# Kernel tuning notes

Hardware: AMD Instinct MI355X
Metric: run time of the kernel (lower is better)

Reference implementation:

```python
import jax, jax.numpy as jnp
import numpy as np
from jax import lax

B, D_MODEL, H, W = 8, 384, 64, 64
D_INNER, D_STATE, D_CONV, DT_RANK = 768, 16, 4, 24
C3, MLP_H = 3 * D_MODEL, 4 * D_MODEL
EPS = 1e-5


def setup_inputs():
    key = jax.random.key(0)
    ks = jax.random.split(key, 16)
    r = lambda i, shape, s=0.02: jax.random.normal(ks[i], shape, jnp.float32) * s
    return {
        'x': jax.random.normal(ks[0], (B, D_MODEL, H, W), jnp.float32),
        'ln1_g': jnp.ones((D_MODEL,), jnp.float32), 'ln1_b': jnp.zeros((D_MODEL,), jnp.float32),
        'in_w': r(1, (2 * D_INNER, D_MODEL)),
        'conv_w': r(2, (D_INNER, 1, D_CONV), 0.2), 'conv_b': jnp.zeros((D_INNER,), jnp.float32),
        'xproj_w': r(3, (DT_RANK + 2 * D_STATE, D_INNER)),
        'dtproj_w': r(4, (D_INNER, DT_RANK), 0.1),
        'dtproj_b': jnp.full((D_INNER,), jnp.log(jnp.expm1(0.01)).item(), jnp.float32),
        'A_log': jnp.log(jnp.broadcast_to(jnp.arange(1, D_STATE + 1, dtype=jnp.float32), (D_INNER, D_STATE))),
        'Dskip': jnp.ones((D_INNER,), jnp.float32),
        'out_w': r(5, (D_MODEL, D_INNER)),
        'dw_w': r(6, (C3, 1, 3, 3), 0.1),
        'bn_g': jnp.ones((C3,), jnp.float32), 'bn_b': jnp.zeros((C3,), jnp.float32),
        'bn_mean': jnp.zeros((C3,), jnp.float32), 'bn_var': jnp.ones((C3,), jnp.float32),
        'pw_w': r(7, (C3, C3)),
        'fus_w': r(8, (D_MODEL, D_MODEL)), 'fus_b': jnp.zeros((D_MODEL,), jnp.float32),
        'ln2_g': jnp.ones((D_MODEL,), jnp.float32), 'ln2_b': jnp.zeros((D_MODEL,), jnp.float32),
        'mlp_w1': r(9, (MLP_H, D_MODEL)), 'mlp_b1': jnp.zeros((MLP_H,), jnp.float32),
        'mlp_w2': r(10, (D_MODEL, MLP_H)), 'mlp_b2': jnp.zeros((D_MODEL,), jnp.float32),
    }


def _ln(x, g, b):
    m = x.mean(-1, keepdims=True)
    v = ((x - m) ** 2).mean(-1, keepdims=True)
    return (x - m) / jnp.sqrt(v + EPS) * g + b


def _dwt(x):
    x01 = x[:, :, 0::2, :] / 2
    x02 = x[:, :, 1::2, :] / 2
    x1, x3 = x01[:, :, :, 0::2], x01[:, :, :, 1::2]
    x2, x4 = x02[:, :, :, 0::2], x02[:, :, :, 1::2]
    ll = x1 + x2 + x3 + x4
    hl = -x1 - x2 + x3 + x4
    lh = -x1 + x2 - x3 + x4
    hh = x1 - x2 - x3 + x4
    return ll, jnp.concatenate([hl, lh, hh], axis=1)


def _idwt(ll, high):
    b, c, h, w = ll.shape
    hl, lh, hh = jnp.split(high, 3, axis=1)
    h_ll, h_hl, h_lh, h_hh = ll / 2, hl / 2, lh / 2, hh / 2
    y1 = h_ll - h_hl - h_lh + h_hh  # (even row, even col)
    y2 = h_ll - h_hl + h_lh - h_hh  # (odd row, even col)
    y3 = h_ll + h_hl - h_lh - h_hh  # (even row, odd col)
    y4 = h_ll + h_hl + h_lh + h_hh  # (odd row, odd col)
    row_e = jnp.stack([y1, y3], axis=-1).reshape(b, c, h, 2 * w)
    row_o = jnp.stack([y2, y4], axis=-1).reshape(b, c, h, 2 * w)
    return jnp.stack([row_e, row_o], axis=-2).reshape(b, c, 2 * h, 2 * w)


def _mamba(x, in_w, conv_w, conv_b, xproj_w, dtproj_w, dtproj_b, A_log, Dskip, out_w):
    # x: [B, L, d_model]
    bb = x.shape[0]
    xz = x @ in_w.T  # [B,L,2*d_inner]
    xi, z = jnp.split(xz, 2, axis=-1)
    xc = jnp.swapaxes(xi, 1, 2)  # [B,d_inner,L]
    xc = lax.conv_general_dilated(xc, conv_w, (1,), [(D_CONV - 1, 0)],
                                  feature_group_count=D_INNER,
                                  dimension_numbers=('NCH', 'OIH', 'NCH')) + conv_b[None, :, None]
    u = jax.nn.silu(jnp.swapaxes(xc, 1, 2))  # [B,L,d_inner]
    dbl = u @ xproj_w.T
    dtr = dbl[..., :DT_RANK]
    Bm = dbl[..., DT_RANK:DT_RANK + D_STATE]
    Cm = dbl[..., DT_RANK + D_STATE:]
    dt = jax.nn.softplus(dtr @ dtproj_w.T + dtproj_b)  # [B,L,d_inner]
    A = -jnp.exp(A_log)  # [d_inner,d_state]

    def step(h, t):
        dt_t, B_t, C_t, u_t = t
        dA = jnp.exp(dt_t[:, :, None] * A)
        h = dA * h + (dt_t * u_t)[:, :, None] * B_t[:, None, :]
        return h, jnp.sum(h * C_t[:, None, :], axis=-1)

    h0 = jnp.zeros((bb, D_INNER, D_STATE), x.dtype)
    xs = (jnp.swapaxes(dt, 0, 1), jnp.swapaxes(Bm, 0, 1), jnp.swapaxes(Cm, 0, 1), jnp.swapaxes(u, 0, 1))
    _, ys = lax.scan(step, h0, xs)
    y = jnp.swapaxes(ys, 0, 1) + u * Dskip
    y = y * jax.nn.silu(z)
    return y @ out_w.T


def reference(x, ln1_g, ln1_b, in_w, conv_w, conv_b, xproj_w, dtproj_w, dtproj_b,
              A_log, Dskip, out_w, dw_w, bn_g, bn_b, bn_mean, bn_var, pw_w,
              fus_w, fus_b, ln2_g, ln2_b, mlp_w1, mlp_b1, mlp_w2, mlp_b2):
    shortcut = x
    x_ll, x_high = _dwt(x)
    b, c, hh, ww = x_ll.shape
    # LL branch: LN -> Mamba -> residual
    x_ll_in = _ln(jnp.transpose(x_ll, (0, 2, 3, 1)), ln1_g, ln1_b)
    y = _mamba(x_ll_in.reshape(b, hh * ww, c), in_w, conv_w, conv_b, xproj_w,
               dtproj_w, dtproj_b, A_log, Dskip, out_w)
    x_ll_out = x_ll + jnp.transpose(y.reshape(b, hh, ww, c), (0, 3, 1, 2))
    # High-freq branch: depthwise3x3 -> BN(eval) -> SiLU -> 1x1 -> residual
    hd = lax.conv_general_dilated(x_high, dw_w, (1, 1), [(1, 1), (1, 1)],
                                  feature_group_count=C3,
                                  dimension_numbers=('NCHW', 'OIHW', 'NCHW'))
    hd = (hd - bn_mean[None, :, None, None]) / jnp.sqrt(bn_var + EPS)[None, :, None, None] \
         * bn_g[None, :, None, None] + bn_b[None, :, None, None]
    hd = jax.nn.silu(hd)
    x_high_out = x_high + jnp.einsum('bchw,oc->bohw', hd, pw_w)
    # Reconstruct + fusion 1x1 conv + residual
    recon = _idwt(x_ll_out, x_high_out)
    recon = jnp.einsum('bchw,oc->bohw', recon, fus_w) + fus_b[None, :, None, None]
    x2 = shortcut + recon
    # LN + MLP + residual
    xn = _ln(jnp.transpose(x2, (0, 2, 3, 1)), ln2_g, ln2_b)
    m = jax.nn.gelu(xn @ mlp_w1.T + mlp_b1, approximate=False) @ mlp_w2.T + mlp_b2
    return x2 + jnp.transpose(m, (0, 3, 1, 2))
```

## Files before the change

### kernel.cpp

```cpp
#include <hip/hip_runtime.h>
#include <hip/hip_bf16.h>
#include <math.h>

typedef __hip_bfloat16 bf16;
typedef __attribute__((ext_vector_type(8))) short bf16x8;
typedef __attribute__((ext_vector_type(4))) float f32x4;
typedef unsigned short u16;

#define LN_EPS 1e-5f

__device__ inline u16 f2b(float v) {
    __hip_bfloat16 h = __float2bfloat16(v);
    return *reinterpret_cast<u16*>(&h);
}

__device__ inline float b2f_lo(unsigned int w) { return __uint_as_float(w << 16); }
__device__ inline float b2f_hi(unsigned int w) { return __uint_as_float(w & 0xFFFF0000u); }

__device__ inline void gload_lds16(const void* g, void* l) {
    __builtin_amdgcn_global_load_lds(
        (const __attribute__((address_space(1))) void*)(uintptr_t)g,
        (__attribute__((address_space(3))) void*)(uintptr_t)(unsigned int)(uintptr_t)l,
        16, 0, 0);
}

__global__ __launch_bounds__(256) void sentinel_kernel(float* __restrict__ out, int n) {
    int i = blockIdx.x * 256 + threadIdx.x;
    if (i < n) out[i] = 123.0f;
}

__global__ __launch_bounds__(256) void reduce12_kernel(const float* __restrict__ P,
                                                       float* __restrict__ out, int n4) {
    int i = blockIdx.x * 256 + threadIdx.x;
    if (i >= n4) return;
    const float4* p4 = (const float4*)P;
    float4 s = p4[i];
#pragma unroll
    for (int z = 1; z < 12; z++) {
        float4 v = p4[(size_t)z * n4 + i];
        s.x += v.x; s.y += v.y; s.z += v.z; s.w += v.w;
    }
    ((float4*)out)[i] = s;
}

__global__ void detect_kernel(const unsigned int* __restrict__ g, int* __restrict__ flag) {
    *flag = (*g == 0x3F803F80u) ? 1 : 0;
}

struct Jobs {
    const void* src[25];
    int prefix[26];
};
__global__ __launch_bounds__(256) void convert_kernel(Jobs J, u16* __restrict__ dst16,
                                                      float* __restrict__ dst32,
                                                      const int* __restrict__ flag) {
    int i = blockIdx.x * 256 + threadIdx.x;
    int total = J.prefix[25];
    if (i >= total) return;
    int f = *flag;
    int lo = 0;
    while (J.prefix[lo + 1] <= i) lo++;
    int off = i - J.prefix[lo];
    float v = f ? (float)((const bf16*)J.src[lo])[off] : ((const float*)J.src[lo])[off];
    if (lo < 6) dst16[i] = f2b(v);
    else        dst32[i - J.prefix[6]] = v;
}

__global__ __launch_bounds__(256) void dwt_kernel(const void* __restrict__ xv,
                                                  float* __restrict__ xll,
                                                  float* __restrict__ xhigh,
                                                  const int* __restrict__ flag) {
    __shared__ float tile[32][133];
    int blk = blockIdx.x;
    int cc = blk % 12;
    int t2 = blk / 12;
    int i  = t2 % 32;
    int b  = t2 / 32;
    int t  = threadIdx.x;
    int c_l = t >> 3;
    int sub = t & 7;
    size_t rowbase = ((size_t)(b * 384 + cc * 32 + c_l)) * 4096 + (size_t)i * 128;
    if (*flag) {
        const u16* xp = (const u16*)xv + rowbase;
#pragma unroll
        for (int k = 0; k < 2; k++) {
            int e0 = (sub + k * 8) * 8;
            uint4 v = *(const uint4*)(xp + e0);
            tile[c_l][e0 + 0] = b2f_lo(v.x); tile[c_l][e0 + 1] = b2f_hi(v.x);
            tile[c_l][e0 + 2] = b2f_lo(v.y); tile[c_l][e0 + 3] = b2f_hi(v.y);
            tile[c_l][e0 + 4] = b2f_lo(v.z); tile[c_l][e0 + 5] = b2f_hi(v.z);
            tile[c_l][e0 + 6] = b2f_lo(v.w); tile[c_l][e0 + 7] = b2f_hi(v.w);
        }
    } else {
        const float* xp = (const float*)xv + rowbase;
#pragma unroll
        for (int k = 0; k < 4; k++) {
            int f0 = (sub + k * 8) * 4;
            float4 v = *(const float4*)(xp + f0);
            tile[c_l][f0 + 0] = v.x; tile[c_l][f0 + 1] = v.y;
            tile[c_l][f0 + 2] = v.z; tile[c_l][f0 + 3] = v.w;
        }
    }
    __syncthreads();
    int c_out = t & 31;
    int jg = t >> 5;
    int cg = cc * 32 + c_out;
#pragma unroll
    for (int jj = 0; jj < 4; jj++) {
        int j = jg * 4 + jj;
        float A = tile[c_out][2 * j];
        float B = tile[c_out][2 * j + 1];
        float C = tile[c_out][64 + 2 * j];
        float D = tile[c_out][64 + 2 * j + 1];
        float ll = 0.5f * (A + B + C + D);
        float hl = 0.5f * (B + D - A - C);
        float lh = 0.5f * (C + D - A - B);
        float hh = 0.5f * (A + D - B - C);
        int pm = b * 1024 + i * 32 + j;
        xll[(size_t)pm * 384 + cg] = ll;
        size_t hb = (size_t)pm * 1152;
        xhigh[hb + cg] = hl;
        xhigh[hb + 384 + cg] = lh;
        xhigh[hb + 768 + cg] = hh;
    }
}

template <bool OBF>
__global__ __launch_bounds__(128) void ln_kernel(const float* __restrict__ in,
                                                 void* __restrict__ outv,
                                                 const float* __restrict__ g,
                                                 const float* __restrict__ b) {
    const int C = 384;
    int row = blockIdx.x;
    int t = threadIdx.x;
    const float* rp = in + (size_t)row * C;
    float v0 = rp[t], v1 = rp[t + 128], v2 = rp[t + 256];
    __shared__ float red[128];
    red[t] = v0 + v1 + v2;
    __syncthreads();
    for (int off = 64; off > 0; off >>= 1) {
        if (t < off) red[t] += red[t + off];
        __syncthreads();
    }
    float mean = red[0] * (1.f / 384.f);
    __syncthreads();
    float d0 = v0 - mean, d1 = v1 - mean, d2 = v2 - mean;
    red[t] = d0 * d0 + d1 * d1 + d2 * d2;
    __syncthreads();
    for (int off = 64; off > 0; off >>= 1) {
        if (t < off) red[t] += red[t + off];
        __syncthreads();
    }
    float inv = rsqrtf(red[0] * (1.f / 384.f) + LN_EPS);
    float o0 = d0 * inv * g[t]       + b[t];
    float o1 = d1 * inv * g[t + 128] + b[t + 128];
    float o2 = d2 * inv * g[t + 256] + b[t + 256];
    if constexpr (OBF) {
        u16* op = (u16*)outv + (size_t)row * C;
        op[t] = f2b(o0); op[t + 128] = f2b(o1); op[t + 256] = f2b(o2);
    } else {
        float* op = (float*)outv + (size_t)row * C;
        op[t] = o0; op[t + 128] = o1; op[t + 256] = o2;
    }
}

#define EP_NONE 0
#define EP_SOFTPLUS_BIAS 1
#define EP_ADD 2
#define EP_FUS 3
#define EP_GELU_BIAS 4
#define EP_FINAL 5

template <int EPIL, bool CBF>
__global__ __launch_bounds__(256) void gemm_mfma(const u16* __restrict__ A, int lda,
                                                 const u16* __restrict__ W,
                                                 void* __restrict__ Cp, int ldc,
                                                 int M, int N, int K,
                                                 const float* __restrict__ addsrc,
                                                 const float* __restrict__ bias,
                                                 const void* __restrict__ xres,
                                                 void* __restrict__ obf,
                                                 int m_off,
                                                 const int* __restrict__ flag) {
    __shared__ u16 Als[2][128][32];
    __shared__ u16 Bls[2][128][32];
    const int t = threadIdx.x;
    const int wave = t >> 6, lane = t & 63;
    const int quad = lane >> 4, r16 = lane & 15;
    const int wm = (wave >> 1) * 64, wn = (wave & 1) * 64;
    const int mb = blockIdx.y * 128, nb = blockIdx.x * 128;
    f32x4 acc[4][4] = {};

    const int srow = wave * 32 + (lane >> 2);
    const int scol = (lane & 3) * 8;
    const u16* Ag0 = A + (size_t)(mb + srow) * lda + scol;
    const u16* Ag1 = A + (size_t)(mb + srow + 16) * lda + scol;
    const u16* Wg0 = W + (size_t)(nb + srow) * (size_t)K + scol;
    const u16* Wg1 = W + (size_t)(nb + srow + 16) * (size_t)K + scol;

    gload_lds16(Ag0, &Als[0][wave * 32][0]);
    gload_lds16(Ag1, &Als[0][wave * 32 + 16][0]);
    gload_lds16(Wg0, &Bls[0][wave * 32][0]);
    gload_lds16(Wg1, &Bls[0][wave * 32 + 16][0]);
    __syncthreads();

    int cur = 0;
    for (int k0 = 0; k0 < K; k0 += 32) {
        int nxt = cur ^ 1;
        if (k0 + 32 < K) {
            gload_lds16(Ag0 + k0 + 32, &Als[nxt][wave * 32][0]);
            gload_lds16(Ag1 + k0 + 32, &Als[nxt][wave * 32 + 16][0]);
            gload_lds16(Wg0 + k0 + 32, &Bls[nxt][wave * 32][0]);
            gload_lds16(Wg1 + k0 + 32, &Bls[nxt][wave * 32 + 16][0]);
        }
        bf16x8 af[4], bfv[4];
#pragma unroll
        for (int i = 0; i < 4; i++) af[i] = *(const bf16x8*)&Als[cur][wm + i * 16 + r16][quad * 8];
#pragma unroll
        for (int j = 0; j < 4; j++) bfv[j] = *(const bf16x8*)&Bls[cur][wn + j * 16 + r16][quad * 8];
#pragma unroll
        for (int i = 0; i < 4; i++)
#pragma unroll
            for (int j = 0; j < 4; j++)
                acc[i][j] = __builtin_amdgcn_mfma_f32_16x16x32_bf16(af[i], bfv[j], acc[i][j], 0, 0, 0);
        __syncthreads();
        cur = nxt;
    }

    int f = 0;
    if constexpr (EPIL == EP_FUS || EPIL == EP_FINAL) f = *flag;
#pragma unroll
    for (int i = 0; i < 4; i++) {
#pragma unroll
        for (int j = 0; j < 4; j++) {
#pragma unroll
            for (int rg = 0; rg < 4; rg++) {
                int m = mb + wm + i * 16 + quad * 4 + rg;
                int n = nb + wn + j * 16 + r16;
                float v = acc[i][j][rg];
                if constexpr (EPIL == EP_NONE) {
                    if constexpr (CBF) ((u16*)Cp)[(size_t)m * ldc + n] = f2b(v);
                    else               ((float*)Cp)[(size_t)m * ldc + n] = v;
                } else if constexpr (EPIL == EP_ADD) {
                    ((float*)Cp)[(size_t)m * ldc + n] = addsrc[(size_t)m * ldc + n] + v;
                } else if constexpr (EPIL == EP_FUS) {
                    v += bias[n];
                    int bb = m >> 12, pix = m & 4095;
                    size_t xi = ((size_t)(bb * 384 + n) << 12) + pix;
                    v += f ? (float)((const bf16*)xres)[xi] : ((const float*)xres)[xi];
                    ((float*)Cp)[(size_t)m * ldc + n] = v;
                } else if constexpr (EPIL == EP_GELU_BIAS) {
                    v += bias[n];
                    v = 0.5f * v * (1.f + erff(v * 0.70710678118654752f));
                    if constexpr (CBF) ((u16*)Cp)[(size_t)m * ldc + n] = f2b(v);
                    else               ((float*)Cp)[(size_t)m * ldc + n] = v;
                } else if constexpr (EPIL == EP_FINAL) {
                    v += bias[n];
                    int gm = m_off + m;
                    v += addsrc[(size_t)gm * 384 + n];
                    int bb = gm >> 12, pix = gm & 4095;
                    size_t oi = ((size_t)(bb * 384 + n) << 12) + pix;
                    if (f) ((bf16*)obf)[oi] = __float2bfloat16(v);
                    else   ((float*)obf)[oi] = v;
                }
            }
        }
    }
}

template <int EPIL, bool SPLITK>
__global__ __launch_bounds__(256) void gemm_nt(const float* __restrict__ A, int lda,
                                               const float* __restrict__ W,
                                               float* __restrict__ C, int ldc,
                                               int M, int N, int K,
                                               const float* __restrict__ bias,
                                               int kc) {
    __shared__ __align__(16) float As[16][68];
    __shared__ __align__(16) float Bs[16][68];
    int t = threadIdx.x;
    int mb = blockIdx.y * 64;
    int nb = blockIdx.x * 64;
    int kb = SPLITK ? blockIdx.z * kc : 0;
    int ke = SPLITK ? kb + kc : K;
    int tm = t & 15, tn = t >> 4;
    float* Cout = C;
    if constexpr (SPLITK) Cout = C + (size_t)blockIdx.z * (size_t)M * ldc;
    float acc[4][4] = {};
    for (int k0 = kb; k0 < ke; k0 += 16) {
#pragma unroll
        for (int i = 0; i < 4; i++) {
            int idx = t + i * 256;
            int r = idx >> 4, c = idx & 15;
            float v = 0.f;
            if (k0 + c < K) v = A[(size_t)(mb + r) * lda + k0 + c];
            As[c][r] = v;
        }
#pragma unroll
        for (int i = 0; i < 4; i++) {
            int idx = t + i * 256;
            int r = idx >> 4, c = idx & 15;
            float v = 0.f;
            if ((nb + r) < N && (k0 + c) < K) v = W[(size_t)(nb + r) * K + k0 + c];
            Bs[c][r] = v;
        }
        __syncthreads();
#pragma unroll
        for (int kk = 0; kk < 16; kk++) {
            float4 av = *(const float4*)&As[kk][tm * 4];
            float4 bv = *(const float4*)&Bs[kk][tn * 4];
            float a4[4] = {av.x, av.y, av.z, av.w};
            float b4[4] = {bv.x, bv.y, bv.z, bv.w};
#pragma unroll
            for (int i = 0; i < 4; i++)
#pragma unroll
                for (int j = 0; j < 4; j++) acc[i][j] += a4[i] * b4[j];
        }
        __syncthreads();
    }
#pragma unroll
    for (int i = 0; i < 4; i++) {
        int m = mb + tm * 4 + i;
        if (m >= M) continue;
#pragma unroll
        for (int j = 0; j < 4; j++) {
            int n = nb + tn * 4 + j;
            if (n >= N) continue;
            float v = acc[i][j];
            if constexpr (SPLITK) {
                Cout[(size_t)m * ldc + n] = v;
            } else if constexpr (EPIL == EP_NONE) {
                C[(size_t)m * ldc + n] = v;
            } else if constexpr (EPIL == EP_SOFTPLUS_BIAS) {
                v += bias[n];
                v = (v > 20.f) ? v : log1pf(expf(v));
                C[(size_t)m * ldc + n] = v;
            }
        }
    }
}

__global__ __launch_bounds__(256) void conv1d_silu_kernel(const float* __restrict__ xz,
                                                          const float* __restrict__ cw,
                                                          const float* __restrict__ cb,
                                                          float* __restrict__ u) {
    int tid = blockIdx.x * 256 + threadIdx.x;
    int dq = tid % 192;
    int t2 = tid / 192;
    int l = t2 % 1024;
    int b = t2 / 1024;
    int d = dq * 4;
    float4 q0 = *(const float4*)&cw[d * 4];
    float4 q1 = *(const float4*)&cw[d * 4 + 4];
    float4 q2 = *(const float4*)&cw[d * 4 + 8];
    float4 q3 = *(const float4*)&cw[d * 4 + 12];
    float4 acc = *(const float4*)&cb[d];
    int rowbase = b * 1024;
#pragma unroll
    for (int k = 0; k < 4; k++) {
        int ls = l - 3 + k;
        if (ls < 0) continue;
        float4 xv = *(const float4*)&xz[(size_t)(rowbase + ls) * 1536 + d];
        acc.x += ((const float*)&q0)[k] * xv.x;
        acc.y += ((const float*)&q1)[k] * xv.y;
        acc.z += ((const float*)&q2)[k] * xv.z;
        acc.w += ((const float*)&q3)[k] * xv.w;
    }
    float4 o;
    o.x = acc.x / (1.f + __expf(-acc.x));
    o.y = acc.y / (1.f + __expf(-acc.y));
    o.z = acc.z / (1.f + __expf(-acc.z));
    o.w = acc.w / (1.f + __expf(-acc.w));
    *(float4*)&u[(size_t)(rowbase + l) * 768 + d] = o;
}

__device__ inline void scan_load_ac(const float* __restrict__ A_log, int d,
                                    float (&Ac)[16], bool& structured) {
#pragma unroll
    for (int s = 0; s < 16; s++) Ac[s] = -__expf(A_log[d * 16 + s]);
    structured = true;
#pragma unroll
    for (int s = 0; s < 16; s++)
        structured = structured && (fabsf(Ac[s] - (s + 1) * Ac[0]) <= 1e-5f * fabsf(Ac[s]));
}

__global__ __launch_bounds__(256) void scan_p1(const float* __restrict__ dt,
                                               const float* __restrict__ u,
                                               const float* __restrict__ dbl,
                                               const float* __restrict__ A_log,
                                               float* __restrict__ st) {
    __shared__ float Bsh[8][16];
    int tloc = threadIdx.x;
    int idx = blockIdx.x * 256 + tloc;
    int g = idx % 6144;
    int c = idx / 6144;
    int d = g % 768, b = g / 768;
    float Ac[16]; bool structured;
    scan_load_ac(A_log, d, Ac, structured);
    float h[16];
#pragma unroll
    for (int s = 0; s < 16; s++) h[s] = 0.f;
    float S = 0.f;
    size_t m0 = (size_t)b * 1024 + c * 128;
    for (int j0 = 0; j0 < 128; j0 += 8) {
        __syncthreads();
        if (tloc < 128) {
            int jj = tloc >> 4, ff = tloc & 15;
            Bsh[jj][ff] = dbl[(m0 + j0 + jj) * 56 + 24 + ff];
        }
        __syncthreads();
        if (structured) {
#pragma unroll
            for (int j = 0; j < 8; j++) {
                size_t m = m0 + j0 + j;
                float dtv = dt[m * 768 + d];
                float uv  = u[m * 768 + d];
                float du = dtv * uv;
                S += dtv;
                float q = __expf(dtv * Ac[0]);
                float a = q;
                h[0] = a * h[0] + du * Bsh[j][0];
#pragma unroll
                for (int s = 1; s < 16; s++) { a *= q; h[s] = a * h[s] + du * Bsh[j][s]; }
            }
        } else {
#pragma unroll
            for (int j = 0; j < 8; j++) {
                size_t m = m0 + j0 + j;
                float dtv = dt[m * 768 + d];
                float uv  = u[m * 768 + d];
                float du = dtv * uv;
                S += dtv;
#pragma unroll
                for (int s = 0; s < 16; s++) h[s] = __expf(dtv * Ac[s]) * h[s] + du * Bsh[j][s];
            }
        }
    }
    float* stp = st + (size_t)(c * 6144 + g) * 32;
#pragma unroll
    for (int s = 0; s < 16; s++) stp[s] = __expf(Ac[s] * S);
#pragma unroll
    for (int s = 0; s < 16; s++) stp[16 + s] = h[s];
}

__global__ __launch_bounds__(256) void scan_p2(float* __restrict__ st) {
    int tid = blockIdx.x * 256 + threadIdx.x;
    int s = tid & 15;
    int g = tid >> 4;
    float H = 0.f;
#pragma unroll
    for (int c = 0; c < 8; c++) {
        size_t i = (size_t)(c * 6144 + g) * 32;
        float P  = st[i + s];
        float hE = st[i + 16 + s];
        st[i + s] = H;
        H = hE + P * H;
    }
}

__global__ __launch_bounds__(256) void scan_p3(const float* __restrict__ dt,
                                               const float* __restrict__ u,
                                               const float* __restrict__ dbl,
                                               const float* __restrict__ z,
                                               const float* __restrict__ A_log,
                                               const float* __restrict__ Dskip,
                                               const float* __restrict__ st,
                                               u16* __restrict__ ybuf) {
    __shared__ float BCsh[8][32];
    int tloc = threadIdx.x;
    int idx = blockIdx.x * 256 + tloc;
    int g = idx % 6144;
    int c = idx / 6144;
    int d = g % 768, b = g / 768;
    float Ac[16]; bool structured;
    scan_load_ac(A_log, d, Ac, structured);
    float Dsk = Dskip[d];
    float h[16];
    const float* stp = st + (size_t)(c * 6144 + g) * 32;
#pragma unroll
    for (int s = 0; s < 16; s++) h[s] = stp[s];
    size_t m0 = (size_t)b * 1024 + c * 128;
    for (int j0 = 0; j0 < 128; j0 += 8) {
        __syncthreads();
        {
            int jj = tloc >> 5, ff = tloc & 31;
            BCsh[jj][ff] = dbl[(m0 + j0 + jj) * 56 + 24 + ff];
        }
        __syncthreads();
        if (structured) {
#pragma unroll
            for (int j = 0; j < 8; j++) {
                size_t m = m0 + j0 + j;
                float dtv = dt[m * 768 + d];
                float uv  = u[m * 768 + d];
                float zv  = z[m * 1536 + 768 + d];
                float du = dtv * uv;
                float q = __expf(dtv * Ac[0]);
                float a = q;
                h[0] = a * h[0] + du * BCsh[j][0];
                float y = h[0] * BCsh[j][16];
#pragma unroll
                for (int s = 1; s < 16; s++) {
                    a *= q;
                    h[s] = a * h[s] + du * BCsh[j][s];
                    y += h[s] * BCsh[j][16 + s];
                }
                float sig = 1.f / (1.f + __expf(-zv));
                ybuf[m * 3072 + d] = f2b((y + uv * Dsk) * (zv * sig));
            }
        } else {
#pragma unroll
            for (int j = 0; j < 8; j++) {
                size_t m = m0 + j0 + j;
                float dtv = dt[m * 768 + d];
                float uv  = u[m * 768 + d];
                float zv  = z[m * 1536 + 768 + d];
                float du = dtv * uv;
                float y = 0.f;
#pragma unroll
                for (int s = 0; s < 16; s++) {
                    h[s] = __expf(dtv * Ac[s]) * h[s] + du * BCsh[j][s];
                    y += h[s] * BCsh[j][16 + s];
                }
                float sig = 1.f / (1.f + __expf(-zv));
                ybuf[m * 3072 + d] = f2b((y + uv * Dsk) * (zv * sig));
            }
        }
    }
}

__global__ __launch_bounds__(256) void dwconv_bn_silu_kernel(const float* __restrict__ xh,
                                                             const float* __restrict__ w,
                                                             const float* __restrict__ g,
                                                             const float* __restrict__ bb,
                                                             const float* __restrict__ mean,
                                                             const float* __restrict__ var,
                                                             u16* __restrict__ hd) {
    int tid = blockIdx.x * 256 + threadIdx.x;
    int cq = tid % 288;
    int t2 = tid / 288;
    int xc = t2 & 3;
    int t3 = t2 >> 2;
    int y = t3 % 32;
    int b = t3 / 32;
    int c = cq * 4;
    float wk[9][4];
#pragma unroll
    for (int i = 0; i < 4; i++) {
        float4 wa = *(const float4*)&w[(c + i) * 9];
        float4 wbv = *(const float4*)&w[(c + i) * 9 + 4];
        float wcv = w[(c + i) * 9 + 8];
        wk[0][i] = wa.x; wk[1][i] = wa.y; wk[2][i] = wa.z; wk[3][i] = wa.w;
        wk[4][i] = wbv.x; wk[5][i] = wbv.y; wk[6][i] = wbv.z; wk[7][i] = wbv.w;
        wk[8][i] = wcv;
    }
    float4 mn = *(const float4*)&mean[c];
    float4 vr = *(const float4*)&var[c];
    float4 gg = *(const float4*)&g[c];
    float4 bv = *(const float4*)&bb[c];
    float scl[4], sft[4];
    scl[0] = rsqrtf(vr.x + LN_EPS) * gg.x; sft[0] = bv.x - mn.x * scl[0];
    scl[1] = rsqrtf(vr.y + LN_EPS) * gg.y; sft[1] = bv.y - mn.y * scl[1];
    scl[2] = rsqrtf(vr.z + LN_EPS) * gg.z; sft[2] = bv.z - mn.z * scl[2];
    scl[3] = rsqrtf(vr.w + LN_EPS) * gg.w; sft[3] = bv.w - mn.w * scl[3];

    int x0 = xc * 8;
    size_t pixbase = (size_t)b * 1024 + y * 32;
    float win[3][3][4];
    auto ldcol = [&](int xx, float (&col)[3][4]) {
#pragma unroll
        for (int r = 0; r < 3; r++) {
            int yy = y + r - 1;
            if (xx < 0 || xx > 31 || yy < 0 || yy > 31) {
                col[r][0] = col[r][1] = col[r][2] = col[r][3] = 0.f;
            } else {
                float4 v = *(const float4*)&xh[((size_t)b * 1024 + yy * 32 + xx) * 1152 + c];
                col[r][0] = v.x; col[r][1] = v.y; col[r][2] = v.z; col[r][3] = v.w;
            }
        }
    };
    ldcol(x0 - 1, win[0]);
    ldcol(x0, win[1]);
#pragma unroll
    for (int xi = 0; xi < 8; xi++) {
        int x = x0 + xi;
        ldcol(x + 1, win[2]);
        ushort4 o;
        u16* op = (u16*)&o;
#pragma unroll
        for (int i = 0; i < 4; i++) {
            float acc = 0.f;
#pragma unroll
            for (int ky = 0; ky < 3; ky++)
#pragma unroll
                for (int kx = 0; kx < 3; kx++)
                    acc += wk[ky * 3 + kx][i] * win[kx][ky][i];
            float vv = acc * scl[i] + sft[i];
            op[i] = f2b(vv / (1.f + __expf(-vv)));
        }
        *(ushort4*)&hd[(pixbase + x) * 1152 + c] = o;
#pragma unroll
        for (int r = 0; r < 3; r++)
#pragma unroll
            for (int i = 0; i < 4; i++) {
                win[0][r][i] = win[1][r][i];
                win[1][r][i] = win[2][r][i];
            }
    }
}

__global__ __launch_bounds__(256) void idwt_kernel(const float* __restrict__ xll,
                                                   const float* __restrict__ xh,
                                                   u16* __restrict__ recon) {
    int idx = blockIdx.x * 256 + threadIdx.x;
    int c = idx % 384;
    int t = idx / 384;
    int p = t % 1024;
    int b = t / 1024;
    int i = p >> 5, j = p & 31;
    float ll = xll[(size_t)(b * 1024 + p) * 384 + c];
    int hb = (b * 1024 + p) * 1152;
    float hl = xh[hb + c];
    float lh = xh[hb + 384 + c];
    float hh = xh[hb + 768 + c];
    float y1 = 0.5f * (ll - hl - lh + hh);
    float y3 = 0.5f * (ll + hl - lh - hh);
    float y2 = 0.5f * (ll - hl + lh - hh);
    float y4 = 0.5f * (ll + hl + lh + hh);
    int r0 = b * 4096 + (2 * i) * 64 + 2 * j;
    recon[(size_t)r0 * 384 + c] = f2b(y1);
    recon[(size_t)(r0 + 1) * 384 + c] = f2b(y3);
    recon[(size_t)(r0 + 64) * 384 + c] = f2b(y2);
    recon[(size_t)(r0 + 65) * 384 + c] = f2b(y4);
}

extern "C" void kernel_launch(void* const* d_in, const int* in_sizes, int n_in,
                              void* d_out, int out_size, void* d_ws, size_t ws_size,
                              hipStream_t stream) {
    const void* x = d_in[0];
    void* out = d_out;

    float* ws = (float*)d_ws;
    float* x_ll    = ws;
    float* x_high  = ws + 3145728;
    u16*   mlp_hid = (u16*)ws;
    float* xz      = ws + 12582912;
    u16*   ybuf    = (u16*)xz;
    u16*   hd      = (u16*)xz;
    u16*   recon   = (u16*)(ws + 17301504);
    u16*   xn      = recon;
    float* u       = ws + 25165824;
    float* dt      = ws + 31457280;
    u16*   x_ll_in = (u16*)dt;
    float* xpart   = dt;
    float* x2      = ws + 25165824;
    float* dbl     = ws + 37748736;
    float* scanst  = ws + 38207488;

    u16* wb16 = (u16*)(ws + 39780352);
    u16* b_in_w   = wb16;
    u16* b_out_w  = wb16 + 589824;
    u16* b_pw_w   = wb16 + 884736;
    u16* b_fus_w  = wb16 + 2211840;
    u16* b_mlp_w1 = wb16 + 2359296;
    u16* b_mlp_w2 = wb16 + 2949120;
    float* f32base = ws + 39780352 + 1769472;
    float* c_conv_w   = f32base;
    float* c_conv_b   = f32base + 3072;
    float* c_xproj_w  = f32base + 3840;
    float* c_dtproj_w = f32base + 46848;
    float* c_dtproj_b = f32base + 65280;
    float* c_A_log    = f32base + 66048;
    float* c_Dskip    = f32base + 78336;
    float* c_dw_w     = f32base + 79104;
    float* c_bn_g     = f32base + 89472;
    float* c_bn_b     = f32base + 90624;
    float* c_bn_mean  = f32base + 91776;
    float* c_bn_var   = f32base + 92928;
    float* c_ln1_g    = f32base + 94080;
    float* c_ln1_b    = f32base + 94464;
    float* c_ln2_g    = f32base + 94848;
    float* c_ln2_b    = f32base + 95232;
    float* c_fus_b    = f32base + 95616;
    float* c_mlp_b1   = f32base + 96000;
    float* c_mlp_b2   = f32base + 97536;
    int* flag = (int*)(f32base + 97920);

    if (ws_size < (size_t)(39780352 + 1769472 + 97920 + 2) * 4) {
        sentinel_kernel<<<(out_size + 255) / 256, 256, 0, stream>>>((float*)out, out_size);
        return;
    }

    detect_kernel<<<1, 1, 0, stream>>>((const unsigned int*)d_in[1], flag);
    Jobs J;
    const int src_idx[25] = {3, 11, 17, 18, 22, 24,
                             4, 5, 6, 7, 8, 9, 10, 12, 13, 14, 15, 16,
                             1, 2, 20, 21, 19, 23, 25};
    const int joff[26] = {0, 589824, 884736, 2211840, 2359296, 2949120, 3538944,
                          3538944 + 3072, 3538944 + 3840, 3538944 + 46848, 3538944 + 65280,
                          3538944 + 66048, 3538944 + 78336, 3538944 + 79104, 3538944 + 89472,
                          3538944 + 90624, 3538944 + 91776, 3538944 + 92928, 3538944 + 94080,
                          3538944 + 94464, 3538944 + 94848, 3538944 + 95232, 3538944 + 95616,
                          3538944 + 96000, 3538944 + 97536, 3538944 + 97920};
    for (int i = 0; i < 25; i++) J.src[i] = d_in[src_idx[i]];
    for (int i = 0; i < 26; i++) J.prefix[i] = joff[i];
    convert_kernel<<<(3636864 + 255) / 256, 256, 0, stream>>>(J, wb16, f32base, flag);

    dwt_kernel<<<3072, 256, 0, stream>>>(x, x_ll, x_high, flag);
    ln_kernel<true><<<8192, 128, 0, stream>>>(x_ll, x_ll_in, c_ln1_g, c_ln1_b);
    gemm_mfma<EP_NONE, false><<<dim3(12, 64), 256, 0, stream>>>(x_ll_in, 384, b_in_w, xz, 1536,
                                                                8192, 1536, 384, nullptr, nullptr, nullptr, nullptr, 0, flag);
    conv1d_silu_kernel<<<6144, 256, 0, stream>>>(xz, c_conv_w, c_conv_b, u);
    gemm_nt<EP_NONE, true><<<dim3(1, 128, 12), 256, 0, stream>>>(u, 768, c_xproj_w, xpart, 56,
                                                                 8192, 56, 768, nullptr, 64);
    reduce12_kernel<<<(114688 + 255) / 256, 256, 0, stream>>>(xpart, dbl, 114688);
    gemm_nt<EP_SOFTPLUS_BIAS, false><<<dim3(12, 128), 256, 0, stream>>>(dbl, 56, c_dtproj_w, dt, 768,
                                                                        8192, 768, 24, c_dtproj_b, 0);
    scan_p1<<<192, 256, 0, stream>>>(dt, u, dbl, c_A_log, scanst);
    scan_p2<<<384, 256, 0, stream>>>(scanst);
    scan_p3<<<192, 256, 0, stream>>>(dt, u, dbl, xz, c_A_log, c_Dskip, scanst, ybuf);
    gemm_mfma<EP_ADD, false><<<dim3(3, 64), 256, 0, stream>>>(ybuf, 3072, b_out_w, x_ll, 384,
                                                              8192, 384, 768, x_ll, nullptr, nullptr, nullptr, 0, flag);
    dwconv_bn_silu_kernel<<<1152, 256, 0, stream>>>(x_high, c_dw_w, c_bn_g, c_bn_b, c_bn_mean, c_bn_var, hd);
    gemm_mfma<EP_ADD, false><<<dim3(9, 64), 256, 0, stream>>>(hd, 1152, b_pw_w, x_high, 1152,
                                                              8192, 1152, 1152, x_high, nullptr, nullptr, nullptr, 0, flag);
    idwt_kernel<<<12288, 256, 0, stream>>>(x_ll, x_high, recon);
    gemm_mfma<EP_FUS, false><<<dim3(3, 256), 256, 0, stream>>>(recon, 384, b_fus_w, x2, 384,
                                                               32768, 384, 384, nullptr, c_fus_b, x, nullptr, 0, flag);
    ln_kernel<true><<<32768, 128, 0, stream>>>(x2, xn, c_ln2_g, c_ln2_b);
    for (int ck = 0; ck < 2; ck++) {
        const u16* xn_c = xn + (size_t)ck * 16384 * 384;
        gemm_mfma<EP_GELU_BIAS, true><<<dim3(12, 128), 256, 0, stream>>>(xn_c, 384, b_mlp_w1, mlp_hid, 1536,
                                                                         16384, 1536, 384, nullptr, c_mlp_b1, nullptr, nullptr, 0, flag);
        gemm_mfma<EP_FINAL, false><<<dim3(3, 128), 256, 0, stream>>>(mlp_hid, 1536, b_mlp_w2, nullptr, 0,
                                                                     16384, 384, 1536, x2, c_mlp_b2, nullptr, out, ck * 16384, flag);
    }
}
```

Before: 758.7 us.

## Split scan state across two lanes, double-buffer B/C via async LDS loads

The scan passes p1 and p3 now give each (batch, channel, chunk) two lanes, each owning 8 of the 16 state entries. This doubles the grid to 384 blocks so more CUs are busy. The B/C coefficients are staged through double-buffered shared memory using global_load_lds prefetch of the next group, and dt/u/z are loaded into registers ahead of compute. The two partial y values are combined with a lane shuffle. In exchange, each dt/u/z value is loaded twice (once per lane) and the chain of power multiplies is longer.

```diff
diff --git a/kernel.cpp b/kernel.cpp
--- a/kernel.cpp
+++ b/kernel.cpp
@@ -22,6 +22,12 @@
         (const __attribute__((address_space(1))) void*)(uintptr_t)g,
         (__attribute__((address_space(3))) void*)(uintptr_t)(unsigned int)(uintptr_t)l,
         16, 0, 0);
+}
+__device__ inline void gload_lds4(const void* g, void* l) {
+    __builtin_amdgcn_global_load_lds(
+        (const __attribute__((address_space(1))) void*)(uintptr_t)g,
+        (__attribute__((address_space(3))) void*)(uintptr_t)(unsigned int)(uintptr_t)l,
+        4, 0, 0);
 }
 
 __global__ __launch_bounds__(256) void sentinel_kernel(float* __restrict__ out, int n) {
@@ -388,58 +394,74 @@
                                                const float* __restrict__ dbl,
                                                const float* __restrict__ A_log,
                                                float* __restrict__ st) {
-    __shared__ float Bsh[8][16];
+    __shared__ float Bsh[2][16][16];
     int tloc = threadIdx.x;
     int idx = blockIdx.x * 256 + tloc;
-    int g = idx % 6144;
-    int c = idx / 6144;
+    int p = idx >> 1;
+    int sh = idx & 1;
+    int g = p % 6144;
+    int c = p / 6144;
     int d = g % 768, b = g / 768;
     float Ac[16]; bool structured;
     scan_load_ac(A_log, d, Ac, structured);
-    float h[16];
-#pragma unroll
-    for (int s = 0; s < 16; s++) h[s] = 0.f;
+    int s0 = sh * 8;
+    float h[8];
+#pragma unroll
+    for (int s = 0; s < 8; s++) h[s] = 0.f;
     float S = 0.f;
     size_t m0 = (size_t)b * 1024 + c * 128;
-    for (int j0 = 0; j0 < 128; j0 += 8) {
-        __syncthreads();
-        if (tloc < 128) {
-            int jj = tloc >> 4, ff = tloc & 15;
-            Bsh[jj][ff] = dbl[(m0 + j0 + jj) * 56 + 24 + ff];
-        }
-        __syncthreads();
+    const int jj = tloc >> 4, ff = tloc & 15;
+    float* lbase0 = &Bsh[0][0][0] + (tloc >> 6) * 64;
+    float* lbase1 = &Bsh[1][0][0] + (tloc >> 6) * 64;
+    gload_lds4(&dbl[(m0 + jj) * 56 + 24 + ff], lbase0);
+    __syncthreads();
+    for (int grp = 0; grp < 8; grp++) {
+        int cur = grp & 1;
+        if (grp + 1 < 8) {
+            gload_lds4(&dbl[(m0 + (grp + 1) * 16 + jj) * 56 + 24 + ff],
+                       cur ? lbase0 : lbase1);
+        }
+        float dtb[16], ub[16];
+#pragma unroll
+        for (int j = 0; j < 16; j++) {
+            size_t m = m0 + grp * 16 + j;
+            dtb[j] = dt[m * 768 + d];
+            ub[j]  = u[m * 768 + d];
+        }
         if (structured) {
 #pragma unroll
-            for (int j = 0; j < 8; j++) {
-                size_t m = m0 + j0 + j;
-                float dtv = dt[m * 768 + d];
-                float uv  = u[m * 768 + d];
-                float du = dtv * uv;
+            for (int j = 0; j < 16; j++) {
+                float dtv = dtb[j];
+                float du = dtv * ub[j];
                 S += dtv;
-                float q = __expf(dtv * Ac[0]);
-                float a = q;
-                h[0] = a * h[0] + du * Bsh[j][0];
-#pragma unroll
-                for (int s = 1; s < 16; s++) { a *= q; h[s] = a * h[s] + du * Bsh[j][s]; }
+                float q  = __expf(dtv * Ac[0]);
+                float q2 = q * q, q3 = q2 * q, q4 = q2 * q2;
+                float q5 = q4 * q, q6 = q4 * q2, q7 = q4 * q3, q8 = q4 * q4;
+                float base = sh ? q8 : 1.f;
+                float a[8] = {base * q,  base * q2, base * q3, base * q4,
+                              base * q5, base * q6, base * q7, base * q8};
+#pragma unroll
+                for (int s = 0; s < 8; s++)
+                    h[s] = a[s] * h[s] + du * Bsh[cur][j][s0 + s];
             }
         } else {
 #pragma unroll
-            for (int j = 0; j < 8; j++) {
-                size_t m = m0 + j0 + j;
-                float dtv = dt[m * 768 + d];
-                float uv  = u[m * 768 + d];
-                float du = dtv * uv;
+            for (int j = 0; j < 16; j++) {
+                float dtv = dtb[j];
+                float du = dtv * ub[j];
                 S += dtv;
 #pragma unroll
-                for (int s = 0; s < 16; s++) h[s] = __expf(dtv * Ac[s]) * h[s] + du * Bsh[j][s];
+                for (int s = 0; s < 8; s++)
+                    h[s] = __expf(dtv * Ac[s0 + s]) * h[s] + du * Bsh[cur][j][s0 + s];
             }
         }
+        __syncthreads();
     }
     float* stp = st + (size_t)(c * 6144 + g) * 32;
 #pragma unroll
-    for (int s = 0; s < 16; s++) stp[s] = __expf(Ac[s] * S);
-#pragma unroll
-    for (int s = 0; s < 16; s++) stp[16 + s] = h[s];
+    for (int s = 0; s < 8; s++) stp[s0 + s] = __expf(Ac[s0 + s] * S);
+#pragma unroll
+    for (int s = 0; s < 8; s++) stp[16 + s0 + s] = h[s];
 }
 
 __global__ __launch_bounds__(256) void scan_p2(float* __restrict__ st) {
@@ -465,66 +487,75 @@
                                                const float* __restrict__ Dskip,
                                                const float* __restrict__ st,
                                                u16* __restrict__ ybuf) {
-    __shared__ float BCsh[8][32];
+    __shared__ float BCsh[2][8][32];
     int tloc = threadIdx.x;
     int idx = blockIdx.x * 256 + tloc;
-    int g = idx % 6144;
-    int c = idx / 6144;
+    int p = idx >> 1;
+    int sh = idx & 1;
+    int g = p % 6144;
+    int c = p / 6144;
     int d = g % 768, b = g / 768;
     float Ac[16]; bool structured;
     scan_load_ac(A_log, d, Ac, structured);
+    int s0 = sh * 8;
     float Dsk = Dskip[d];
-    float h[16];
+    float h[8];
     const float* stp = st + (size_t)(c * 6144 + g) * 32;
 #pragma unroll
-    for (int s = 0; s < 16; s++) h[s] = stp[s];
+    for (int s = 0; s < 8; s++) h[s] = stp[s0 + s];
     size_t m0 = (size_t)b * 1024 + c * 128;
-    for (int j0 = 0; j0 < 128; j0 += 8) {
-        __syncthreads();
-        {
-            int jj = tloc >> 5, ff = tloc & 31;
-            BCsh[jj][ff] = dbl[(m0 + j0 + jj) * 56 + 24 + ff];
-        }
-        __syncthreads();
-        if (structured) {
-#pragma unroll
-            for (int j = 0; j < 8; j++) {
-                size_t m = m0 + j0 + j;
-                float dtv = dt[m * 768 + d];
-                float uv  = u[m * 768 + d];
-                float zv  = z[m * 1536 + 768 + d];
-                float du = dtv * uv;
-                float q = __expf(dtv * Ac[0]);
-                float a = q;
-                h[0] = a * h[0] + du * BCsh[j][0];
-                float y = h[0] * BCsh[j][16];
-#pragma unroll
-                for (int s = 1; s < 16; s++) {
-                    a *= q;
-                    h[s] = a * h[s] + du * BCsh[j][s];
-                    y += h[s] * BCsh[j][16 + s];
-                }
+    const int jj = tloc >> 5, ff = tloc & 31;
+    float* lbase0 = &BCsh[0][0][0] + (tloc >> 6) * 64;
+    float* lbase1 = &BCsh[1][0][0] + (tloc >> 6) * 64;
+    gload_lds4(&dbl[(m0 + jj) * 56 + 24 + ff], lbase0);
+    __syncthreads();
+    for (int grp = 0; grp < 16; grp++) {
+        int cur = grp & 1;
+        if (grp + 1 < 16) {
+            gload_lds4(&dbl[(m0 + (grp + 1) * 8 + jj) * 56 + 24 + ff],
+                       cur ? lbase0 : lbase1);
+        }
+        float dtb[8], ub[8], zb[8];
+#pragma unroll
+        for (int j = 0; j < 8; j++) {
+            size_t m = m0 + grp * 8 + j;
+            dtb[j] = dt[m * 768 + d];
+            ub[j]  = u[m * 768 + d];
+            zb[j]  = z[m * 1536 + 768 + d];
+        }
+#pragma unroll
+        for (int j = 0; j < 8; j++) {
+            size_t m = m0 + grp * 8 + j;
+            float dtv = dtb[j];
+            float uv  = ub[j];
+            float zv  = zb[j];
+            float du = dtv * uv;
+            if (structured) {
+                float q  = __expf(dtv * Ac[0]);
+                float q2 = q * q, q3 = q2 * q, q4 = q2 * q2;
+                float q5 = q4 * q, q6 = q4 * q2, q7 = q4 * q3, q8 = q4 * q4;
+                float base = sh ? q8 : 1.f;
+                float a[8] = {base * q,  base * q2, base * q3, base * q4,
+                              base * q5, base * q6, base * q7, base * q8};
+#pragma unroll
+                for (int s = 0; s < 8; s++)
+                    h[s] = a[s] * h[s] + du * BCsh[cur][j][s0 + s];
+            } else {
+#pragma unroll
+                for (int s = 0; s < 8; s++)
+                    h[s] = __expf(dtv * Ac[s0 + s]) * h[s] + du * BCsh[cur][j][s0 + s];
+            }
+            float pr[8];
+#pragma unroll
+            for (int s = 0; s < 8; s++) pr[s] = h[s] * BCsh[cur][j][16 + s0 + s];
+            float y = ((pr[0] + pr[1]) + (pr[2] + pr[3])) + ((pr[4] + pr[5]) + (pr[6] + pr[7]));
+            y += __shfl_xor(y, 1);
+            if (!sh) {
                 float sig = 1.f / (1.f + __expf(-zv));
                 ybuf[m * 3072 + d] = f2b((y + uv * Dsk) * (zv * sig));
             }
-        } else {
-#pragma unroll
-            for (int j = 0; j < 8; j++) {
-                size_t m = m0 + j0 + j;
-                float dtv = dt[m * 768 + d];
-                float uv  = u[m * 768 + d];
-                float zv  = z[m * 1536 + 768 + d];
-                float du = dtv * uv;
-                float y = 0.f;
-#pragma unroll
-                for (int s = 0; s < 16; s++) {
-                    h[s] = __expf(dtv * Ac[s]) * h[s] + du * BCsh[j][s];
-                    y += h[s] * BCsh[j][16 + s];
-                }
-                float sig = 1.f / (1.f + __expf(-zv));
-                ybuf[m * 3072 + d] = f2b((y + uv * Dsk) * (zv * sig));
-            }
-        }
+        }
+        __syncthreads();
     }
 }
 
@@ -715,9 +746,9 @@
     reduce12_kernel<<<(114688 + 255) / 256, 256, 0, stream>>>(xpart, dbl, 114688);
     gemm_nt<EP_SOFTPLUS_BIAS, false><<<dim3(12, 128), 256, 0, stream>>>(dbl, 56, c_dtproj_w, dt, 768,
                                                                         8192, 768, 24, c_dtproj_b, 0);
-    scan_p1<<<192, 256, 0, stream>>>(dt, u, dbl, c_A_log, scanst);
+    scan_p1<<<384, 256, 0, stream>>>(dt, u, dbl, c_A_log, scanst);
     scan_p2<<<384, 256, 0, stream>>>(scanst);
-    scan_p3<<<192, 256, 0, stream>>>(dt, u, dbl, xz, c_A_log, c_Dskip, scanst, ybuf);
+    scan_p3<<<384, 256, 0, stream>>>(dt, u, dbl, xz, c_A_log, c_Dskip, scanst, ybuf);
     gemm_mfma<EP_ADD, false><<<dim3(3, 64), 256, 0, stream>>>(ybuf, 3072, b_out_w, x_ll, 384,
                                                               8192, 384, 768, x_ll, nullptr, nullptr, nullptr, 0, flag);
     dwconv_bn_silu_kernel<<<1152, 256, 0, stream>>>(x_high, c_dw_w, c_bn_g, c_bn_b, c_bn_mean, c_bn_var, hd);
```

New measurement: 735.2 us. 3.1% less time.
